# Kernel tuning notes

Measured on AMD Instinct MI355X. Metric: run time of the kernel, lower is better.

The kernel has to match this reference:

```python
import jax, jax.numpy as jnp
import numpy as np

B, S, D, H = 2, 2048, 1024, 16
W = D // H  # head width = 64


def setup_inputs() -> dict:
    key = jax.random.key(0)
    ks = jax.random.split(key, 10)
    std = 1.0 / np.sqrt(D)
    return {
        "x": jax.random.normal(ks[0], (B, S, D), jnp.float32),
        "seg": jax.random.randint(ks[1], (B, S), 0, 2, jnp.int64),
        "Wq": jax.random.normal(ks[2], (D, D), jnp.float32) * std,
        "bq": jnp.zeros((D,), jnp.float32),
        "Wk": jax.random.normal(ks[3], (D, D), jnp.float32) * std,
        "bk": jnp.zeros((D,), jnp.float32),
        "Wv": jax.random.normal(ks[4], (D, D), jnp.float32) * std,
        "bv": jnp.zeros((D,), jnp.float32),
        "Wo": jax.random.normal(ks[5], (D, D), jnp.float32) * std,
        "bo": jnp.zeros((D,), jnp.float32),
    }


def reference(x, seg, Wq, bq, Wk, bk, Wv, bv, Wo, bo):
    # QKV projections: (B,S,D)
    q = x @ Wq + bq
    k = x @ Wk + bk
    v = x @ Wv + bv
    # split heads -> (B,H,S,W)
    def heads(t):
        return t.reshape(B, S, H, W).transpose(0, 2, 1, 3)
    q, k, v = heads(q), heads(k), heads(v)
    scale = 1.0 / np.sqrt(W).astype(np.float32)
    scores = jnp.einsum("bhqw,bhkw->bhqk", q, k) * scale  # (B,H,S,S)
    # causal mask: strictly-upper-triangular entries -> -inf
    causal = jnp.tril(jnp.ones((S, S), dtype=bool))
    scores = jnp.where(causal, scores, -jnp.inf)
    attn = jax.nn.softmax(scores, axis=-1)
    h = jnp.einsum("bhqk,bhkw->bhqw", attn, v)  # (B,H,S,W)
    h = h.transpose(0, 2, 1, 3).reshape(B, S, D)  # merge heads
    return h @ Wo + bo
```

## Files before the change

kernel.cpp:

```cpp
#include <hip/hip_runtime.h>

#define BB 2
#define SS 2048
#define DD 1024
#define HH 16
#define WW 64
#define MM (BB*SS)

typedef float f32x4 __attribute__((ext_vector_type(4)));
typedef short s16x8 __attribute__((ext_vector_type(8)));
typedef short s16x4 __attribute__((ext_vector_type(4)));

__device__ __forceinline__ unsigned short f2bf(float f) {
  return __builtin_bit_cast(unsigned short, (__bf16)f);
}
__device__ __forceinline__ float bf2f(unsigned short u) {
  return (float)__builtin_bit_cast(__bf16, u);
}
__device__ __forceinline__ void dma16(const unsigned short* g, unsigned short* l) {
  __builtin_amdgcn_global_load_lds(
      (const __attribute__((address_space(1))) unsigned int*)g,
      (__attribute__((address_space(3))) unsigned int*)l, 16, 0, 0);
}

__global__ __launch_bounds__(256) void k_prep(const float* __restrict__ x,
                                              unsigned short* __restrict__ xb,
                                              const float* __restrict__ W0,
                                              const float* __restrict__ W1,
                                              const float* __restrict__ W2,
                                              const float* __restrict__ W3,
                                              unsigned short* __restrict__ T0,
                                              unsigned short* __restrict__ T1,
                                              unsigned short* __restrict__ T2,
                                              unsigned short* __restrict__ T3) {
  if (blockIdx.z >= 4) {
    int blk = (blockIdx.z - 4) * 1024 + blockIdx.y * 32 + blockIdx.x;
    int i = (blk * 256 + threadIdx.x) * 4;
    float4 v = *(const float4*)(x + i);
    *(ushort4*)(xb + i) = make_ushort4(f2bf(v.x), f2bf(v.y), f2bf(v.z), f2bf(v.w));
    return;
  }
  const float* Wm = blockIdx.z == 0 ? W0 : blockIdx.z == 1 ? W1 : blockIdx.z == 2 ? W2 : W3;
  unsigned short* Wt = blockIdx.z == 0 ? T0 : blockIdx.z == 1 ? T1 : blockIdx.z == 2 ? T2 : T3;
  __shared__ float tile[32][33];
  int bn = blockIdx.x * 32;
  int bk = blockIdx.y * 32;
  int tx = threadIdx.x & 31;
  int ty = threadIdx.x >> 5;
#pragma unroll
  for (int r = 0; r < 4; ++r)
    tile[ty + r * 8][tx] = Wm[(bk + ty + r * 8) * DD + bn + tx];
  __syncthreads();
#pragma unroll
  for (int r = 0; r < 4; ++r)
    Wt[(bn + ty + r * 8) * DD + bk + tx] = f2bf(tile[tx][ty + r * 8]);
}

__global__ __launch_bounds__(256, 3) void k_gemm_qkv(const unsigned short* __restrict__ A,
                                                     const unsigned short* __restrict__ Wcat,
                                                     const float* __restrict__ bq,
                                                     const float* __restrict__ bk,
                                                     const float* __restrict__ bv,
                                                     unsigned short* __restrict__ Qo,
                                                     unsigned short* __restrict__ Ko,
                                                     unsigned short* __restrict__ Vo) {
  __shared__ __align__(16) unsigned short As[2][128 * 32];
  __shared__ __align__(16) unsigned short Bs[2][128 * 32];
  const int widx = blockIdx.x >> 3;
  const int n0 = (blockIdx.x & 7) * 128;
  const int m0 = blockIdx.y * 128;
  const unsigned short* Bt = Wcat + (size_t)widx * DD * DD;
  const float* bias = widx == 0 ? bq : widx == 1 ? bk : bv;
  unsigned short* outp = widx == 0 ? Qo : widx == 1 ? Ko : Vo;
  const float oscale = widx == 0 ? 0.125f * 1.4426950408889634f : 1.0f;
  const int t = threadIdx.x;
  const int wv = t >> 6, lane = t & 63;
  const int quad = lane >> 4, l16 = lane & 15;
  const int wm = (wv >> 1) * 64, wn = (wv & 1) * 64;
  const unsigned short* srcA[2];
  const unsigned short* srcB[2];
  int dstoff[2];
#pragma unroll
  for (int d = 0; d < 2; ++d) {
    int s = d * 256 + wv * 64 + lane;
    int r = s >> 2, pb = s & 3;
    int lc = ((pb ^ (r & 3)) << 3);
    srcA[d] = A + (size_t)(m0 + r) * DD + lc;
    srcB[d] = Bt + (size_t)(n0 + r) * DD + lc;
    dstoff[d] = (d * 256 + wv * 64) * 8;
  }
  f32x4 acc[4][4] = {};

#pragma unroll
  for (int d = 0; d < 2; ++d) {
    dma16(srcA[d], &As[0][dstoff[d]]);
    dma16(srcB[d], &Bs[0][dstoff[d]]);
  }

  for (int it = 0; it < DD / 32; ++it) {
    asm volatile("s_waitcnt vmcnt(0)" ::: "memory");
    __syncthreads();
    if (it + 1 < DD / 32) {
      const int nb = (it + 1) & 1;
      const int k1 = (it + 1) * 32;
#pragma unroll
      for (int d = 0; d < 2; ++d) {
        dma16(srcA[d] + k1, &As[nb][dstoff[d]]);
        dma16(srcB[d] + k1, &Bs[nb][dstoff[d]]);
      }
    }
    const unsigned short* Asb = As[it & 1];
    const unsigned short* Bsb = Bs[it & 1];
    s16x8 af[4], bfr[4];
#pragma unroll
    for (int mi = 0; mi < 4; ++mi) {
      int ra = wm + mi * 16 + l16;
      af[mi] = *(const s16x8*)(Asb + ra * 32 + ((quad ^ (ra & 3)) << 3));
    }
#pragma unroll
    for (int ni = 0; ni < 4; ++ni) {
      int rb = wn + ni * 16 + l16;
      bfr[ni] = *(const s16x8*)(Bsb + rb * 32 + ((quad ^ (rb & 3)) << 3));
    }
#pragma unroll
    for (int mi = 0; mi < 4; ++mi)
#pragma unroll
      for (int ni = 0; ni < 4; ++ni)
        acc[mi][ni] = __builtin_amdgcn_mfma_f32_16x16x32_bf16(af[mi], bfr[ni], acc[mi][ni], 0, 0, 0);
  }

#pragma unroll
  for (int mi = 0; mi < 4; ++mi) {
#pragma unroll
    for (int ni = 0; ni < 4; ++ni) {
      int col = n0 + wn + ni * 16 + l16;
      float bb = bias[col];
      int h = col >> 6, w = col & 63;
#pragma unroll
      for (int r = 0; r < 4; ++r) {
        int row = m0 + wm + mi * 16 + quad * 4 + r;
        float v = (acc[mi][ni][r] + bb) * oscale;
        int b = row >> 11, s = row & (SS - 1);
        long off;
        if (widx == 2) off = (long)(b * HH + h) * (SS * WW) + (long)w * SS + s;
        else           off = (long)(b * HH + h) * (SS * WW) + (long)s * WW + w;
        outp[off] = f2bf(v);
      }
    }
  }
}

__global__ __launch_bounds__(256, 3) void k_gemm_out(const unsigned short* __restrict__ A,
                                                     const unsigned short* __restrict__ Bt,
                                                     const float* __restrict__ bias,
                                                     float* __restrict__ out_f) {
  __shared__ __align__(16) unsigned short As[2][128 * 32];
  __shared__ __align__(16) unsigned short Bs[2][64 * 32];
  const int m0 = blockIdx.y * 128, n0 = blockIdx.x * 64;
  const int t = threadIdx.x;
  const int wv = t >> 6, lane = t & 63;
  const int quad = lane >> 4, l16 = lane & 15;
  const int wm = (wv >> 1) * 64, wn = (wv & 1) * 32;
  const unsigned short* srcA[2];
  int dstA[2];
#pragma unroll
  for (int d = 0; d < 2; ++d) {
    int s = d * 256 + wv * 64 + lane;
    int r = s >> 2, pb = s & 3;
    int lc = ((pb ^ (r & 3)) << 3);
    srcA[d] = A + (size_t)(m0 + r) * DD + lc;
    dstA[d] = (d * 256 + wv * 64) * 8;
  }
  const int sB = wv * 64 + lane;
  const int rB = sB >> 2, pbB = sB & 3;
  const unsigned short* srcB = Bt + (size_t)(n0 + rB) * DD + ((pbB ^ (rB & 3)) << 3);
  const int dstB = (wv * 64) * 8;
  f32x4 acc[4][2] = {};

#pragma unroll
  for (int d = 0; d < 2; ++d) dma16(srcA[d], &As[0][dstA[d]]);
  dma16(srcB, &Bs[0][dstB]);

  for (int it = 0; it < DD / 32; ++it) {
    asm volatile("s_waitcnt vmcnt(0)" ::: "memory");
    __syncthreads();
    if (it + 1 < DD / 32) {
      const int nb = (it + 1) & 1;
      const int k1 = (it + 1) * 32;
#pragma unroll
      for (int d = 0; d < 2; ++d) dma16(srcA[d] + k1, &As[nb][dstA[d]]);
      dma16(srcB + k1, &Bs[nb][dstB]);
    }
    const unsigned short* Asb = As[it & 1];
    const unsigned short* Bsb = Bs[it & 1];
    s16x8 af[4], bfr[2];
#pragma unroll
    for (int mi = 0; mi < 4; ++mi) {
      int ra = wm + mi * 16 + l16;
      af[mi] = *(const s16x8*)(Asb + ra * 32 + ((quad ^ (ra & 3)) << 3));
    }
#pragma unroll
    for (int ni = 0; ni < 2; ++ni) {
      int rb = wn + ni * 16 + l16;
      bfr[ni] = *(const s16x8*)(Bsb + rb * 32 + ((quad ^ (rb & 3)) << 3));
    }
#pragma unroll
    for (int mi = 0; mi < 4; ++mi)
#pragma unroll
      for (int ni = 0; ni < 2; ++ni)
        acc[mi][ni] = __builtin_amdgcn_mfma_f32_16x16x32_bf16(af[mi], bfr[ni], acc[mi][ni], 0, 0, 0);
  }

#pragma unroll
  for (int mi = 0; mi < 4; ++mi)
#pragma unroll
    for (int ni = 0; ni < 2; ++ni) {
      int col = n0 + wn + ni * 16 + l16;
      float bb = bias[col];
#pragma unroll
      for (int r = 0; r < 4; ++r) {
        int row = m0 + wm + mi * 16 + quad * 4 + r;
        out_f[row * DD + col] = acc[mi][ni][r] + bb;
      }
    }
}

__global__ __launch_bounds__(256, 2) void k_attn_mfma(const unsigned short* __restrict__ Q,
                                                      const unsigned short* __restrict__ K,
                                                      const unsigned short* __restrict__ Vt,
                                                      unsigned short* __restrict__ hm) {
  __shared__ __align__(16) unsigned short Kbuf[2][128 * 64];
  __shared__ __align__(16) unsigned short Vbuf[2][64 * 128];
  const int id = blockIdx.y * 16 + blockIdx.x;
  const int xcd = id & 7;
  const int j = id >> 3;
  const int bh = xcd * 4 + (j & 3);
  const int px = j >> 2;
  const int pairp = px >> 1;
  const int qh = px & 1;
  const int t = threadIdx.x;
  const int wv = t >> 6, lane = t & 63;
  const int quad = lane >> 4, l16 = lane & 15;
  const unsigned short* Qp = Q + (size_t)bh * SS * WW;
  const unsigned short* Kp = K + (size_t)bh * SS * WW;
  const unsigned short* Vp = Vt + (size_t)bh * WW * SS;
  const int b = bh >> 4, h = bh & 15;

  const int rrK = lane >> 3;
  const int kswz = (((lane & 7) ^ rrK) << 3);

  for (int sp = 0; sp < 2; ++sp) {
    const int strip = sp == 0 ? pairp : 15 - pairp;
    const int qs = strip * 128;
    const int qb = qs + qh * 64 + wv * 16;

    s16x8 qf[2];
#pragma unroll
    for (int c = 0; c < 2; ++c)
      qf[c] = *(const s16x8*)(Qp + (qb + l16) * WW + c * 32 + quad * 8);

    f32x4 O[4] = {};
    float l = 0.f;

    const int nkt = strip + 1;

#pragma unroll
    for (int d = 0; d < 4; ++d) {
      const int D = wv * 4 + d;
      dma16(Kp + (size_t)(D * 8 + rrK) * WW + kswz, &Kbuf[0][D * 512]);
      const int vrow = D * 4 + quad;
      dma16(Vp + (size_t)vrow * SS + (((lane & 15) ^ (vrow & 7)) << 3), &Vbuf[0][D * 512]);
    }

    for (int kt = 0; kt < nkt; ++kt) {
      const int kb = kt * 128;
      asm volatile("s_waitcnt vmcnt(0)" ::: "memory");
      __syncthreads();
      if (kt + 1 < nkt) {
        const int nb = (kt + 1) & 1;
        const int kbn = kb + 128;
#pragma unroll
        for (int d = 0; d < 4; ++d) {
          const int D = wv * 4 + d;
          dma16(Kp + (size_t)(kbn + D * 8 + rrK) * WW + kswz, &Kbuf[nb][D * 512]);
          const int vrow = D * 4 + quad;
          dma16(Vp + (size_t)vrow * SS + kbn + (((lane & 15) ^ (vrow & 7)) << 3),
                &Vbuf[nb][D * 512]);
        }
      }
      const unsigned short* Kb_ = Kbuf[kt & 1];
      const unsigned short* Vb_ = Vbuf[kt & 1];

      s16x8 kf[8][2];
#pragma unroll
      for (int mt = 0; mt < 8; ++mt)
#pragma unroll
        for (int c = 0; c < 2; ++c)
          kf[mt][c] = *(const s16x8*)(Kb_ + (mt * 16 + l16) * 64 + (((c * 4 + quad) ^ (l16 & 7)) << 3));

      f32x4 sc[8] = {};
      __builtin_amdgcn_s_setprio(1);
#pragma unroll
      for (int mt = 0; mt < 8; ++mt)
#pragma unroll
        for (int c = 0; c < 2; ++c)
          sc[mt] = __builtin_amdgcn_mfma_f32_16x16x32_bf16(kf[mt][c], qf[c], sc[mt], 0, 0, 0);
      __builtin_amdgcn_s_setprio(0);

      if (kt == nkt - 1) {
#pragma unroll
        for (int mt = 0; mt < 8; ++mt)
#pragma unroll
          for (int r = 0; r < 4; ++r)
            if (kb + mt * 16 + quad * 4 + r > qb + l16)
              sc[mt][r] = -__builtin_inff();
      }

#pragma unroll
      for (int mt = 0; mt < 8; ++mt)
#pragma unroll
        for (int r = 0; r < 4; ++r)
          sc[mt][r] = __builtin_amdgcn_exp2f(sc[mt][r]);

      s16x8 pf[4];
#pragma unroll
      for (int c = 0; c < 4; ++c) {
#pragma unroll
        for (int e = 0; e < 4; ++e) {
          pf[c][e]     = (short)f2bf(sc[2 * c][e]);
          pf[c][4 + e] = (short)f2bf(sc[2 * c + 1][e]);
        }
      }

      float ts[8];
#pragma unroll
      for (int mt = 0; mt < 8; ++mt)
        ts[mt] = (sc[mt][0] + sc[mt][1]) + (sc[mt][2] + sc[mt][3]);
      l += ((ts[0] + ts[1]) + (ts[2] + ts[3])) + ((ts[4] + ts[5]) + (ts[6] + ts[7]));

      const int xr = l16 & 7;
      __builtin_amdgcn_s_setprio(1);
#pragma unroll
      for (int ni = 0; ni < 4; ++ni) {
        const unsigned short* vrp = Vb_ + (ni * 16 + l16) * 128 + ((quad & 1) << 2);
#pragma unroll
        for (int c = 0; c < 4; ++c) {
          const int blo = (4 * c + (quad >> 1)) ^ xr;
          const int bhi = (4 * c + 2 + (quad >> 1)) ^ xr;
          s16x4 vlo = *(const s16x4*)(vrp + (blo << 3));
          s16x4 vhi = *(const s16x4*)(vrp + (bhi << 3));
          s16x8 vfc = __builtin_shufflevector(vlo, vhi, 0, 1, 2, 3, 4, 5, 6, 7);
          O[ni] = __builtin_amdgcn_mfma_f32_16x16x32_bf16(pf[c], vfc, O[ni], 0, 0, 0);
        }
      }
      __builtin_amdgcn_s_setprio(0);
    }

    l += __shfl_xor(l, 16);
    l += __shfl_xor(l, 32);
#pragma unroll
    for (int r = 0; r < 4; ++r) {
      const float linv = 1.f / __shfl(l, quad * 4 + r);
      const int q = qb + quad * 4 + r;
#pragma unroll
      for (int ni = 0; ni < 4; ++ni)
        hm[(size_t)(b * SS + q) * DD + h * WW + ni * 16 + l16] = f2bf(O[ni][r] * linv);
    }
    __syncthreads();
  }
}

extern "C" void kernel_launch(void* const* d_in, const int* in_sizes, int n_in,
                              void* d_out, int out_size, void* d_ws, size_t ws_size,
                              hipStream_t stream) {
  const float* x  = (const float*)d_in[0];
  const float* Wq = (const float*)d_in[2];
  const float* bq = (const float*)d_in[3];
  const float* Wk = (const float*)d_in[4];
  const float* bk = (const float*)d_in[5];
  const float* Wv = (const float*)d_in[6];
  const float* bv = (const float*)d_in[7];
  const float* Wo = (const float*)d_in[8];
  const float* bo = (const float*)d_in[9];
  float* out = (float*)d_out;

  char* ws = (char*)d_ws;
  unsigned short* xb   = (unsigned short*)(ws);
  unsigned short* Wcat = (unsigned short*)(ws + (size_t)( 8 << 20));
  unsigned short* Wtq  = Wcat;
  unsigned short* Wtk  = Wcat + (size_t)DD * DD;
  unsigned short* Wtv  = Wcat + (size_t)2 * DD * DD;
  unsigned short* Wto  = (unsigned short*)(ws + (size_t)(14 << 20));
  unsigned short* Qb   = (unsigned short*)(ws + (size_t)(16 << 20));
  unsigned short* Kb   = (unsigned short*)(ws + (size_t)(24 << 20));
  unsigned short* Vtb  = (unsigned short*)(ws + (size_t)(32 << 20));
  unsigned short* hm   = (unsigned short*)(ws + (size_t)(40 << 20));

  dim3 pg(32, 32, 8);
  k_prep<<<pg, 256, 0, stream>>>(x, xb, Wq, Wk, Wv, Wo, Wtq, Wtk, Wtv, Wto);

  dim3 gq(24, MM / 128);
  k_gemm_qkv<<<gq, 256, 0, stream>>>(xb, Wcat, bq, bk, bv, Qb, Kb, Vtb);

  dim3 ag(16, BB * HH);
  k_attn_mfma<<<ag, 256, 0, stream>>>(Qb, Kb, Vtb, hm);

  dim3 go(DD / 64, MM / 128);
  k_gemm_out<<<go, 256, 0, stream>>>(hm, Wto, bo, out);
}
```

Baseline: 188.3 us.

## Fuse attention and output projection into one persistent kernel with grid barrier

Merges the attention kernel and the output-projection GEMM into a single 512-block kernel that shares one 64KB LDS buffer. A software grid-wide barrier built on atomics separates the two phases, so the output GEMM starts only after all attention rows have been written. This removes one kernel launch and the idle gap between them. In exchange, every block waits at the barrier, the GEMM now runs at 2 blocks per CU instead of 3, and correctness depends on all 512 blocks being resident at once.

```diff
diff --git a/kernel.cpp b/kernel.cpp
--- a/kernel.cpp
+++ b/kernel.cpp
@@ -14,13 +14,31 @@
 __device__ __forceinline__ unsigned short f2bf(float f) {
   return __builtin_bit_cast(unsigned short, (__bf16)f);
 }
-__device__ __forceinline__ float bf2f(unsigned short u) {
-  return (float)__builtin_bit_cast(__bf16, u);
-}
 __device__ __forceinline__ void dma16(const unsigned short* g, unsigned short* l) {
   __builtin_amdgcn_global_load_lds(
       (const __attribute__((address_space(1))) unsigned int*)g,
       (__attribute__((address_space(3))) unsigned int*)l, 16, 0, 0);
+}
+
+__device__ unsigned g_count = 0;
+__device__ unsigned g_gen = 0;
+
+__device__ __forceinline__ void grid_sync512() {
+  __syncthreads();
+  if (threadIdx.x == 0) {
+    __threadfence();
+    unsigned gen = __hip_atomic_load(&g_gen, __ATOMIC_RELAXED, __HIP_MEMORY_SCOPE_AGENT);
+    unsigned n = __hip_atomic_fetch_add(&g_count, 1u, __ATOMIC_RELAXED, __HIP_MEMORY_SCOPE_AGENT);
+    if (n + 1u == 512u) {
+      __hip_atomic_store(&g_count, 0u, __ATOMIC_RELAXED, __HIP_MEMORY_SCOPE_AGENT);
+      __hip_atomic_store(&g_gen, gen + 1u, __ATOMIC_RELEASE, __HIP_MEMORY_SCOPE_AGENT);
+    } else {
+      while (__hip_atomic_load(&g_gen, __ATOMIC_RELAXED, __HIP_MEMORY_SCOPE_AGENT) == gen)
+        __builtin_amdgcn_s_sleep(32);
+    }
+    __threadfence();
+  }
+  __syncthreads();
 }
 
 __global__ __launch_bounds__(256) void k_prep(const float* __restrict__ x,
@@ -150,223 +168,221 @@
   }
 }
 
-__global__ __launch_bounds__(256, 3) void k_gemm_out(const unsigned short* __restrict__ A,
-                                                     const unsigned short* __restrict__ Bt,
-                                                     const float* __restrict__ bias,
-                                                     float* __restrict__ out_f) {
-  __shared__ __align__(16) unsigned short As[2][128 * 32];
-  __shared__ __align__(16) unsigned short Bs[2][64 * 32];
-  const int m0 = blockIdx.y * 128, n0 = blockIdx.x * 64;
+__global__ __launch_bounds__(256, 2) void k_attn_out(
+    const unsigned short* __restrict__ Q, const unsigned short* __restrict__ K,
+    const unsigned short* __restrict__ Vt, unsigned short* __restrict__ hm,
+    const unsigned short* __restrict__ Wto, const float* __restrict__ bo,
+    float* __restrict__ out) {
+  __shared__ __align__(16) unsigned char smem[65536];
+  const int blk = blockIdx.x;
   const int t = threadIdx.x;
-  const int wv = t >> 6, lane = t & 63;
+  const int wvi = t >> 6, lane = t & 63;
   const int quad = lane >> 4, l16 = lane & 15;
-  const int wm = (wv >> 1) * 64, wn = (wv & 1) * 32;
-  const unsigned short* srcA[2];
-  int dstA[2];
-#pragma unroll
-  for (int d = 0; d < 2; ++d) {
-    int s = d * 256 + wv * 64 + lane;
-    int r = s >> 2, pb = s & 3;
-    int lc = ((pb ^ (r & 3)) << 3);
-    srcA[d] = A + (size_t)(m0 + r) * DD + lc;
-    dstA[d] = (d * 256 + wv * 64) * 8;
-  }
-  const int sB = wv * 64 + lane;
-  const int rB = sB >> 2, pbB = sB & 3;
-  const unsigned short* srcB = Bt + (size_t)(n0 + rB) * DD + ((pbB ^ (rB & 3)) << 3);
-  const int dstB = (wv * 64) * 8;
-  f32x4 acc[4][2] = {};
-
-#pragma unroll
-  for (int d = 0; d < 2; ++d) dma16(srcA[d], &As[0][dstA[d]]);
-  dma16(srcB, &Bs[0][dstB]);
-
-  for (int it = 0; it < DD / 32; ++it) {
-    asm volatile("s_waitcnt vmcnt(0)" ::: "memory");
-    __syncthreads();
-    if (it + 1 < DD / 32) {
-      const int nb = (it + 1) & 1;
-      const int k1 = (it + 1) * 32;
-#pragma unroll
-      for (int d = 0; d < 2; ++d) dma16(srcA[d] + k1, &As[nb][dstA[d]]);
-      dma16(srcB + k1, &Bs[nb][dstB]);
-    }
-    const unsigned short* Asb = As[it & 1];
-    const unsigned short* Bsb = Bs[it & 1];
-    s16x8 af[4], bfr[2];
-#pragma unroll
-    for (int mi = 0; mi < 4; ++mi) {
-      int ra = wm + mi * 16 + l16;
-      af[mi] = *(const s16x8*)(Asb + ra * 32 + ((quad ^ (ra & 3)) << 3));
-    }
-#pragma unroll
-    for (int ni = 0; ni < 2; ++ni) {
-      int rb = wn + ni * 16 + l16;
-      bfr[ni] = *(const s16x8*)(Bsb + rb * 32 + ((quad ^ (rb & 3)) << 3));
-    }
-#pragma unroll
-    for (int mi = 0; mi < 4; ++mi)
-#pragma unroll
-      for (int ni = 0; ni < 2; ++ni)
-        acc[mi][ni] = __builtin_amdgcn_mfma_f32_16x16x32_bf16(af[mi], bfr[ni], acc[mi][ni], 0, 0, 0);
-  }
-
-#pragma unroll
-  for (int mi = 0; mi < 4; ++mi)
-#pragma unroll
-    for (int ni = 0; ni < 2; ++ni) {
-      int col = n0 + wn + ni * 16 + l16;
-      float bb = bias[col];
+
+  {
+    unsigned short* Ksh = (unsigned short*)smem;
+    unsigned short* Vsh = (unsigned short*)(smem + 32768);
+    const int xcd = blk & 7;
+    const int j = blk >> 3;
+    const int bh = xcd * 4 + (j & 3);
+    const int px = j >> 2;
+    const int pairp = px >> 1;
+    const int qh = px & 1;
+    const unsigned short* Qp = Q + (size_t)bh * SS * WW;
+    const unsigned short* Kp = K + (size_t)bh * SS * WW;
+    const unsigned short* Vp = Vt + (size_t)bh * WW * SS;
+    const int b = bh >> 4, h = bh & 15;
+    const int rrK = lane >> 3;
+    const int kswz = (((lane & 7) ^ rrK) << 3);
+
+    for (int sp = 0; sp < 2; ++sp) {
+      const int strip = sp == 0 ? pairp : 15 - pairp;
+      const int qs = strip * 128;
+      const int qb = qs + qh * 64 + wvi * 16;
+
+      s16x8 qf[2];
+#pragma unroll
+      for (int c = 0; c < 2; ++c)
+        qf[c] = *(const s16x8*)(Qp + (qb + l16) * WW + c * 32 + quad * 8);
+
+      f32x4 O[4] = {};
+      float l = 0.f;
+      const int nkt = strip + 1;
+
+#pragma unroll
+      for (int d = 0; d < 4; ++d) {
+        const int D = wvi * 4 + d;
+        dma16(Kp + (size_t)(D * 8 + rrK) * WW + kswz, Ksh + D * 512);
+        const int vrow = D * 4 + quad;
+        dma16(Vp + (size_t)vrow * SS + (((lane & 15) ^ (vrow & 7)) << 3), Vsh + D * 512);
+      }
+
+      for (int kt = 0; kt < nkt; ++kt) {
+        const int kb = kt * 128;
+        asm volatile("s_waitcnt vmcnt(0)" ::: "memory");
+        __syncthreads();
+        if (kt + 1 < nkt) {
+          const int nb = (kt + 1) & 1;
+          const int kbn = kb + 128;
+#pragma unroll
+          for (int d = 0; d < 4; ++d) {
+            const int D = wvi * 4 + d;
+            dma16(Kp + (size_t)(kbn + D * 8 + rrK) * WW + kswz, Ksh + nb * 8192 + D * 512);
+            const int vrow = D * 4 + quad;
+            dma16(Vp + (size_t)vrow * SS + kbn + (((lane & 15) ^ (vrow & 7)) << 3),
+                  Vsh + nb * 8192 + D * 512);
+          }
+        }
+        const unsigned short* Kb_ = Ksh + (kt & 1) * 8192;
+        const unsigned short* Vb_ = Vsh + (kt & 1) * 8192;
+
+        s16x8 kf[8][2];
+#pragma unroll
+        for (int mt = 0; mt < 8; ++mt)
+#pragma unroll
+          for (int c = 0; c < 2; ++c)
+            kf[mt][c] = *(const s16x8*)(Kb_ + (mt * 16 + l16) * 64 + (((c * 4 + quad) ^ (l16 & 7)) << 3));
+
+        f32x4 sc[8] = {};
+        __builtin_amdgcn_s_setprio(1);
+#pragma unroll
+        for (int mt = 0; mt < 8; ++mt)
+#pragma unroll
+          for (int c = 0; c < 2; ++c)
+            sc[mt] = __builtin_amdgcn_mfma_f32_16x16x32_bf16(kf[mt][c], qf[c], sc[mt], 0, 0, 0);
+        __builtin_amdgcn_s_setprio(0);
+
+        if (kt == nkt - 1) {
+#pragma unroll
+          for (int mt = 0; mt < 8; ++mt)
+#pragma unroll
+            for (int r = 0; r < 4; ++r)
+              if (kb + mt * 16 + quad * 4 + r > qb + l16)
+                sc[mt][r] = -__builtin_inff();
+        }
+
+#pragma unroll
+        for (int mt = 0; mt < 8; ++mt)
+#pragma unroll
+          for (int r = 0; r < 4; ++r)
+            sc[mt][r] = __builtin_amdgcn_exp2f(sc[mt][r]);
+
+        s16x8 pf[4];
+#pragma unroll
+        for (int c = 0; c < 4; ++c) {
+#pragma unroll
+          for (int e = 0; e < 4; ++e) {
+            pf[c][e]     = (short)f2bf(sc[2 * c][e]);
+            pf[c][4 + e] = (short)f2bf(sc[2 * c + 1][e]);
+          }
+        }
+
+        float ts[8];
+#pragma unroll
+        for (int mt = 0; mt < 8; ++mt)
+          ts[mt] = (sc[mt][0] + sc[mt][1]) + (sc[mt][2] + sc[mt][3]);
+        l += ((ts[0] + ts[1]) + (ts[2] + ts[3])) + ((ts[4] + ts[5]) + (ts[6] + ts[7]));
+
+        const int xr = l16 & 7;
+        __builtin_amdgcn_s_setprio(1);
+#pragma unroll
+        for (int ni = 0; ni < 4; ++ni) {
+          const unsigned short* vrp = Vb_ + (ni * 16 + l16) * 128 + ((quad & 1) << 2);
+#pragma unroll
+          for (int c = 0; c < 4; ++c) {
+            const int blo = (4 * c + (quad >> 1)) ^ xr;
+            const int bhi = (4 * c + 2 + (quad >> 1)) ^ xr;
+            s16x4 vlo = *(const s16x4*)(vrp + (blo << 3));
+            s16x4 vhi = *(const s16x4*)(vrp + (bhi << 3));
+            s16x8 vfc = __builtin_shufflevector(vlo, vhi, 0, 1, 2, 3, 4, 5, 6, 7);
+            O[ni] = __builtin_amdgcn_mfma_f32_16x16x32_bf16(pf[c], vfc, O[ni], 0, 0, 0);
+          }
+        }
+        __builtin_amdgcn_s_setprio(0);
+      }
+
+      l += __shfl_xor(l, 16);
+      l += __shfl_xor(l, 32);
 #pragma unroll
       for (int r = 0; r < 4; ++r) {
-        int row = m0 + wm + mi * 16 + quad * 4 + r;
-        out_f[row * DD + col] = acc[mi][ni][r] + bb;
-      }
-    }
-}
-
-__global__ __launch_bounds__(256, 2) void k_attn_mfma(const unsigned short* __restrict__ Q,
-                                                      const unsigned short* __restrict__ K,
-                                                      const unsigned short* __restrict__ Vt,
-                                                      unsigned short* __restrict__ hm) {
-  __shared__ __align__(16) unsigned short Kbuf[2][128 * 64];
-  __shared__ __align__(16) unsigned short Vbuf[2][64 * 128];
-  const int id = blockIdx.y * 16 + blockIdx.x;
-  const int xcd = id & 7;
-  const int j = id >> 3;
-  const int bh = xcd * 4 + (j & 3);
-  const int px = j >> 2;
-  const int pairp = px >> 1;
-  const int qh = px & 1;
-  const int t = threadIdx.x;
-  const int wv = t >> 6, lane = t & 63;
-  const int quad = lane >> 4, l16 = lane & 15;
-  const unsigned short* Qp = Q + (size_t)bh * SS * WW;
-  const unsigned short* Kp = K + (size_t)bh * SS * WW;
-  const unsigned short* Vp = Vt + (size_t)bh * WW * SS;
-  const int b = bh >> 4, h = bh & 15;
-
-  const int rrK = lane >> 3;
-  const int kswz = (((lane & 7) ^ rrK) << 3);
-
-  for (int sp = 0; sp < 2; ++sp) {
-    const int strip = sp == 0 ? pairp : 15 - pairp;
-    const int qs = strip * 128;
-    const int qb = qs + qh * 64 + wv * 16;
-
-    s16x8 qf[2];
-#pragma unroll
-    for (int c = 0; c < 2; ++c)
-      qf[c] = *(const s16x8*)(Qp + (qb + l16) * WW + c * 32 + quad * 8);
-
-    f32x4 O[4] = {};
-    float l = 0.f;
-
-    const int nkt = strip + 1;
-
-#pragma unroll
-    for (int d = 0; d < 4; ++d) {
-      const int D = wv * 4 + d;
-      dma16(Kp + (size_t)(D * 8 + rrK) * WW + kswz, &Kbuf[0][D * 512]);
-      const int vrow = D * 4 + quad;
-      dma16(Vp + (size_t)vrow * SS + (((lane & 15) ^ (vrow & 7)) << 3), &Vbuf[0][D * 512]);
-    }
-
-    for (int kt = 0; kt < nkt; ++kt) {
-      const int kb = kt * 128;
+        const float linv = 1.f / __shfl(l, quad * 4 + r);
+        const int q = qb + quad * 4 + r;
+#pragma unroll
+        for (int ni = 0; ni < 4; ++ni)
+          hm[(size_t)(b * SS + q) * DD + h * WW + ni * 16 + l16] = f2bf(O[ni][r] * linv);
+      }
+      __syncthreads();
+    }
+  }
+  grid_sync512();
+
+  {
+    unsigned short* As = (unsigned short*)smem;
+    unsigned short* Bs = (unsigned short*)(smem + 16384);
+    const int m0 = (blk >> 4) * 128, n0 = (blk & 15) * 64;
+    const int wm = (wvi >> 1) * 64, wn = (wvi & 1) * 32;
+    const unsigned short* srcA[2];
+    int dstA[2];
+#pragma unroll
+    for (int d = 0; d < 2; ++d) {
+      int s = d * 256 + wvi * 64 + lane;
+      int r = s >> 2, pb = s & 3;
+      int lc = ((pb ^ (r & 3)) << 3);
+      srcA[d] = hm + (size_t)(m0 + r) * DD + lc;
+      dstA[d] = (d * 256 + wvi * 64) * 8;
+    }
+    const int sB = wvi * 64 + lane;
+    const int rB = sB >> 2, pbB = sB & 3;
+    const unsigned short* srcB = Wto + (size_t)(n0 + rB) * DD + ((pbB ^ (rB & 3)) << 3);
+    const int dstB = (wvi * 64) * 8;
+    f32x4 acc[4][2] = {};
+
+#pragma unroll
+    for (int d = 0; d < 2; ++d) dma16(srcA[d], As + dstA[d]);
+    dma16(srcB, Bs + dstB);
+
+    for (int it = 0; it < DD / 32; ++it) {
       asm volatile("s_waitcnt vmcnt(0)" ::: "memory");
       __syncthreads();
-      if (kt + 1 < nkt) {
-        const int nb = (kt + 1) & 1;
-        const int kbn = kb + 128;
-#pragma unroll
-        for (int d = 0; d < 4; ++d) {
-          const int D = wv * 4 + d;
-          dma16(Kp + (size_t)(kbn + D * 8 + rrK) * WW + kswz, &Kbuf[nb][D * 512]);
-          const int vrow = D * 4 + quad;
-          dma16(Vp + (size_t)vrow * SS + kbn + (((lane & 15) ^ (vrow & 7)) << 3),
-                &Vbuf[nb][D * 512]);
+      if (it + 1 < DD / 32) {
+        const int nb = (it + 1) & 1;
+        const int k1 = (it + 1) * 32;
+#pragma unroll
+        for (int d = 0; d < 2; ++d) dma16(srcA[d] + k1, As + nb * 4096 + dstA[d]);
+        dma16(srcB + k1, Bs + nb * 2048 + dstB);
+      }
+      const unsigned short* Asb = As + (it & 1) * 4096;
+      const unsigned short* Bsb = Bs + (it & 1) * 2048;
+      s16x8 af[4], bfr[2];
+#pragma unroll
+      for (int mi = 0; mi < 4; ++mi) {
+        int ra = wm + mi * 16 + l16;
+        af[mi] = *(const s16x8*)(Asb + ra * 32 + ((quad ^ (ra & 3)) << 3));
+      }
+#pragma unroll
+      for (int ni = 0; ni < 2; ++ni) {
+        int rb = wn + ni * 16 + l16;
+        bfr[ni] = *(const s16x8*)(Bsb + rb * 32 + ((quad ^ (rb & 3)) << 3));
+      }
+#pragma unroll
+      for (int mi = 0; mi < 4; ++mi)
+#pragma unroll
+        for (int ni = 0; ni < 2; ++ni)
+          acc[mi][ni] = __builtin_amdgcn_mfma_f32_16x16x32_bf16(af[mi], bfr[ni], acc[mi][ni], 0, 0, 0);
+    }
+
+#pragma unroll
+    for (int mi = 0; mi < 4; ++mi)
+#pragma unroll
+      for (int ni = 0; ni < 2; ++ni) {
+        int col = n0 + wn + ni * 16 + l16;
+        float bb = bo[col];
+#pragma unroll
+        for (int r = 0; r < 4; ++r) {
+          int row = m0 + wm + mi * 16 + quad * 4 + r;
+          out[(size_t)row * DD + col] = acc[mi][ni][r] + bb;
         }
       }
-      const unsigned short* Kb_ = Kbuf[kt & 1];
-      const unsigned short* Vb_ = Vbuf[kt & 1];
-
-      s16x8 kf[8][2];
-#pragma unroll
-      for (int mt = 0; mt < 8; ++mt)
-#pragma unroll
-        for (int c = 0; c < 2; ++c)
-          kf[mt][c] = *(const s16x8*)(Kb_ + (mt * 16 + l16) * 64 + (((c * 4 + quad) ^ (l16 & 7)) << 3));
-
-      f32x4 sc[8] = {};
-      __builtin_amdgcn_s_setprio(1);
-#pragma unroll
-      for (int mt = 0; mt < 8; ++mt)
-#pragma unroll
-        for (int c = 0; c < 2; ++c)
-          sc[mt] = __builtin_amdgcn_mfma_f32_16x16x32_bf16(kf[mt][c], qf[c], sc[mt], 0, 0, 0);
-      __builtin_amdgcn_s_setprio(0);
-
-      if (kt == nkt - 1) {
-#pragma unroll
-        for (int mt = 0; mt < 8; ++mt)
-#pragma unroll
-          for (int r = 0; r < 4; ++r)
-            if (kb + mt * 16 + quad * 4 + r > qb + l16)
-              sc[mt][r] = -__builtin_inff();
-      }
-
-#pragma unroll
-      for (int mt = 0; mt < 8; ++mt)
-#pragma unroll
-        for (int r = 0; r < 4; ++r)
-          sc[mt][r] = __builtin_amdgcn_exp2f(sc[mt][r]);
-
-      s16x8 pf[4];
-#pragma unroll
-      for (int c = 0; c < 4; ++c) {
-#pragma unroll
-        for (int e = 0; e < 4; ++e) {
-          pf[c][e]     = (short)f2bf(sc[2 * c][e]);
-          pf[c][4 + e] = (short)f2bf(sc[2 * c + 1][e]);
-        }
-      }
-
-      float ts[8];
-#pragma unroll
-      for (int mt = 0; mt < 8; ++mt)
-        ts[mt] = (sc[mt][0] + sc[mt][1]) + (sc[mt][2] + sc[mt][3]);
-      l += ((ts[0] + ts[1]) + (ts[2] + ts[3])) + ((ts[4] + ts[5]) + (ts[6] + ts[7]));
-
-      const int xr = l16 & 7;
-      __builtin_amdgcn_s_setprio(1);
-#pragma unroll
-      for (int ni = 0; ni < 4; ++ni) {
-        const unsigned short* vrp = Vb_ + (ni * 16 + l16) * 128 + ((quad & 1) << 2);
-#pragma unroll
-        for (int c = 0; c < 4; ++c) {
-          const int blo = (4 * c + (quad >> 1)) ^ xr;
-          const int bhi = (4 * c + 2 + (quad >> 1)) ^ xr;
-          s16x4 vlo = *(const s16x4*)(vrp + (blo << 3));
-          s16x4 vhi = *(const s16x4*)(vrp + (bhi << 3));
-          s16x8 vfc = __builtin_shufflevector(vlo, vhi, 0, 1, 2, 3, 4, 5, 6, 7);
-          O[ni] = __builtin_amdgcn_mfma_f32_16x16x32_bf16(pf[c], vfc, O[ni], 0, 0, 0);
-        }
-      }
-      __builtin_amdgcn_s_setprio(0);
-    }
-
-    l += __shfl_xor(l, 16);
-    l += __shfl_xor(l, 32);
-#pragma unroll
-    for (int r = 0; r < 4; ++r) {
-      const float linv = 1.f / __shfl(l, quad * 4 + r);
-      const int q = qb + quad * 4 + r;
-#pragma unroll
-      for (int ni = 0; ni < 4; ++ni)
-        hm[(size_t)(b * SS + q) * DD + h * WW + ni * 16 + l16] = f2bf(O[ni][r] * linv);
-    }
-    __syncthreads();
   }
 }
 
@@ -402,9 +418,5 @@
   dim3 gq(24, MM / 128);
   k_gemm_qkv<<<gq, 256, 0, stream>>>(xb, Wcat, bq, bk, bv, Qb, Kb, Vtb);
 
-  dim3 ag(16, BB * HH);
-  k_attn_mfma<<<ag, 256, 0, stream>>>(Qb, Kb, Vtb, hm);
-
-  dim3 go(DD / 64, MM / 128);
-  k_gemm_out<<<go, 256, 0, stream>>>(hm, Wto, bo, out);
-}
+  k_attn_out<<<dim3(512), dim3(256), 0, stream>>>(Qb, Kb, Vtb, hm, Wto, bo, out);
+}
```

Result: slower. 241.6 us (+28.3%).
